# Kernel tuning notes

Hardware: AMD Instinct MI355X
Metric: run time of the kernel (lower is better)

## Reference

```python
import jax, jax.numpy as jnp
import numpy as np

N = 20000
E = 320000
IN_DIM = 16
H = 128
HEADS = 4
NEG_SLOPE = 0.2  # GATv2Conv default
EPS_LN = 1e-5


def setup_inputs() -> dict:
    key = jax.random.key(0)
    ks = jax.random.split(key, 16)
    f32 = jnp.float32
    def rn(k, shape, scale):
        return jax.random.normal(k, shape, dtype=f32) * scale
    s_in = 1.0 / np.sqrt(IN_DIM)
    s_h = 1.0 / np.sqrt(H)
    s_4h = 1.0 / np.sqrt(4 * H)
    s_2h = 1.0 / np.sqrt(2 * H)
    inp = {}
    inp["x"] = jax.random.normal(ks[0], (N, IN_DIM), dtype=f32)
    inp["edge_index"] = jax.random.randint(ks[1], (2, E), 0, N)
    inp["edge_attr"] = jax.random.normal(ks[2], (E, 2), dtype=f32)
    inp["emb_w"] = rn(ks[3], (IN_DIM, H), s_in)
    inp["emb_b"] = jnp.zeros((H,), f32)
    # 3 GATv2 layers stacked on leading axis
    inp["lin_l"] = rn(ks[4], (3, H, HEADS * H), s_h)
    inp["lin_r"] = rn(ks[5], (3, H, HEADS * H), s_h)
    inp["lin_edge"] = rn(ks[6], (3, 2, HEADS * H), 1.0 / np.sqrt(2.0))
    inp["att"] = rn(ks[7], (3, HEADS, H), s_h)
    inp["conv_bias01"] = jnp.zeros((2, HEADS * H), f32)  # concat=True layers
    inp["conv_bias2"] = jnp.zeros((H,), f32)             # concat=False layer
    inp["proj_w"] = rn(ks[8], (2, HEADS * H, H), s_4h)
    inp["proj_b"] = jnp.zeros((2, H), f32)
    inp["n1_g"] = jnp.ones((3, H), f32)
    inp["n1_b"] = jnp.zeros((3, H), f32)
    inp["n2_g"] = jnp.ones((3, H), f32)
    inp["n2_b"] = jnp.zeros((3, H), f32)
    inp["ffn_w1"] = rn(ks[9], (3, H, 2 * H), s_h)
    inp["ffn_b1"] = jnp.zeros((3, 2 * H), f32)
    inp["ffn_w2"] = rn(ks[10], (3, 2 * H, H), s_2h)
    inp["ffn_b2"] = jnp.zeros((3, H), f32)
    return inp


def layer_norm(x, g, b):
    mu = jnp.mean(x, axis=-1, keepdims=True)
    var = jnp.mean((x - mu) ** 2, axis=-1, keepdims=True)
    return (x - mu) * jax.lax.rsqrt(var + EPS_LN) * g + b


def gatv2(h, src, dst, eattr, Wl, Wr, We, att, bias, concat, n):
    # h: [n, H]; per-edge gather -> GATv2 attention -> segment softmax -> scatter-add
    xl = (h @ Wl).reshape(n, HEADS, H)   # source transform
    xr = (h @ Wr).reshape(n, HEADS, H)   # target transform
    ee = (eattr @ We).reshape(-1, HEADS, H)
    e = jax.nn.leaky_relu(xl[src] + xr[dst] + ee, NEG_SLOPE)  # [E', HEADS, H]
    score = jnp.einsum('ehc,hc->eh', e, att)                  # [E', HEADS]
    smax = jax.ops.segment_max(score, dst, num_segments=n)
    p = jnp.exp(score - smax[dst])
    denom = jax.ops.segment_sum(p, dst, num_segments=n)
    alpha = p / (denom[dst] + 1e-16)
    out = jax.ops.segment_sum(xl[src] * alpha[..., None], dst, num_segments=n)
    if concat:
        return out.reshape(n, HEADS * H) + bias
    return jnp.mean(out, axis=1) + bias


def reference(x, edge_index, edge_attr, emb_w, emb_b, lin_l, lin_r, lin_edge, att,
              conv_bias01, conv_bias2, proj_w, proj_b, n1_g, n1_b, n2_g, n2_b,
              ffn_w1, ffn_b1, ffn_w2, ffn_b2):
    n = x.shape[0]
    e = edge_attr.shape[0]
    # PyG add_self_loops with fill_value='mean': self-loop attr = mean of incoming edge attrs
    ones = jnp.ones((e,), x.dtype)
    deg = jax.ops.segment_sum(ones, edge_index[1], num_segments=n)
    loop_attr = jax.ops.segment_sum(edge_attr, edge_index[1], num_segments=n) / jnp.maximum(deg, 1.0)[:, None]
    ar = jnp.arange(n)
    src = jnp.concatenate([edge_index[0], ar])
    dst = jnp.concatenate([edge_index[1], ar])
    ea = jnp.concatenate([edge_attr, loop_attr], axis=0)

    h = x @ emb_w + emb_b
    for i in range(3):
        concat = i < 2
        bias = conv_bias01[i] if concat else conv_bias2
        h_in = h
        h = gatv2(h, src, dst, ea, lin_l[i], lin_r[i], lin_edge[i], att[i], bias, concat, n)
        if concat:
            h = h @ proj_w[i] + proj_b[i]
        h = layer_norm(h + h_in, n1_g[i], n1_b[i])
        h2 = h
        h = jax.nn.gelu(h @ ffn_w1[i] + ffn_b1[i], approximate=False) @ ffn_w2[i] + ffn_b2[i]
        h = layer_norm(h + h2, n2_g[i], n2_b[i])
    return h
```

## Files before the change

kernel.cpp:

```cpp
#include <hip/hip_runtime.h>
#include <math.h>

#define IN_DIM 16
#define HDIM   128
#define HEADS  4
#define HH     512
#define FFH    256
#define NEG_SLOPE 0.2f

typedef _Float16 half8 __attribute__((ext_vector_type(8)));
typedef _Float16 h8 __attribute__((ext_vector_type(8)));
typedef _Float16 h4 __attribute__((ext_vector_type(4)));
typedef _Float16 h2 __attribute__((ext_vector_type(2)));
typedef float f32x4 __attribute__((ext_vector_type(4)));

struct __align__(8) Edge { int src; _Float16 ea0, ea1; };

static __device__ inline float hsum8(h8 v) {
    h4 a = __builtin_shufflevector(v, v, 0, 1, 2, 3) +
           __builtin_shufflevector(v, v, 4, 5, 6, 7);
    h2 b = __builtin_shufflevector(a, a, 0, 1) +
           __builtin_shufflevector(a, a, 2, 3);
    return (float)b[0] + (float)b[1];
}

__global__ void xpad_kernel(const float* __restrict__ x, _Float16* __restrict__ xh, int n) {
    int idx = blockIdx.x * 256 + threadIdx.x;
    if (idx >= n * 64) return;
    int r = idx >> 6, k = idx & 63;
    xh[idx] = (k < IN_DIM) ? (_Float16)x[r * IN_DIM + k] : (_Float16)0.0f;
}

struct WDesc { const float* src; _Float16* dst; int Ksrc; int lgKd; int lgN; };
struct WDescs { WDesc d[15]; };
__global__ void wconv_kernel(WDescs ds) {
    WDesc w = ds.d[blockIdx.y];
    int Kd = 1 << w.lgKd;
    int total = 1 << (w.lgKd + w.lgN);
    for (int idx = blockIdx.x * 256 + threadIdx.x; idx < total; idx += gridDim.x * 256) {
        int n2 = idx >> w.lgKd, k = idx & (Kd - 1);
        w.dst[idx] = (k < w.Ksrc) ? (_Float16)w.src[(k << w.lgN) + n2] : (_Float16)0.0f;
    }
}

__global__ void wcvt_kernel(const float* __restrict__ we, const float* __restrict__ att,
                            const float* __restrict__ cb,
                            _Float16* __restrict__ weh, _Float16* __restrict__ atth,
                            _Float16* __restrict__ cbh) {
    int i = blockIdx.x * 256 + threadIdx.x;
    if (i < 3072) weh[i] = (_Float16)we[i];
    else if (i < 4608) atth[i - 3072] = (_Float16)att[i - 3072];
    else if (i < 5632) cbh[i - 4608] = (_Float16)cb[i - 4608];
}

__global__ void deg_kernel(const int* __restrict__ ei, const float* __restrict__ eattr,
                           float* deg, float* asum, int E) {
    int e = blockIdx.x * blockDim.x + threadIdx.x;
    if (e >= E) return;
    int d = ei[E + e];
    atomicAdd(&deg[d], 1.0f);
    atomicAdd(&asum[2 * d], eattr[2 * e]);
    atomicAdd(&asum[2 * d + 1], eattr[2 * e + 1]);
}

__global__ void scan_kernel(const float* __restrict__ deg, int* row_ptr, int* cur, int n) {
    __shared__ int sums[1024];
    int tid = threadIdx.x;
    int per = (n + 1023) / 1024;
    int s0 = tid * per;
    int s1 = s0 + per; if (s1 > n) s1 = n;
    int s = 0;
    for (int i = s0; i < s1; i++) s += (int)deg[i] + 1;
    int mysum = s;
    sums[tid] = s;
    __syncthreads();
    for (int dd = 1; dd < 1024; dd <<= 1) {
        int t = (tid >= dd) ? sums[tid - dd] : 0;
        __syncthreads();
        sums[tid] += t;
        __syncthreads();
    }
    int run = sums[tid] - mysum;
    for (int i = s0; i < s1; i++) {
        row_ptr[i] = run; cur[i] = run;
        run += (int)deg[i] + 1;
    }
    if (tid == 1023) row_ptr[n] = sums[1023];
}

__global__ void scatter_kernel(const int* __restrict__ ei, const float* __restrict__ eattr,
                               const float* __restrict__ deg, const float* __restrict__ asum,
                               int* cur, Edge* csr, int E, int n) {
    int i = blockIdx.x * blockDim.x + threadIdx.x;
    if (i >= E + n) return;
    Edge ed;
    int pos;
    if (i < E) {
        int d = ei[E + i];
        pos = atomicAdd(&cur[d], 1);
        ed.src = ei[i];
        ed.ea0 = (_Float16)eattr[2 * i];
        ed.ea1 = (_Float16)eattr[2 * i + 1];
    } else {
        int nd = i - E;
        float dv = fmaxf(deg[nd], 1.0f);
        pos = atomicAdd(&cur[nd], 1);
        ed.src = nd;
        ed.ea0 = (_Float16)(asum[2 * nd] / dv);
        ed.ea1 = (_Float16)(asum[2 * nd + 1] / dv);
    }
    csr[pos] = ed;
}

template <int KT, int OUTMODE>
__global__ __launch_bounds__(256) void gemm_bstat(const _Float16* __restrict__ A, int lda,
                                                  const _Float16* __restrict__ BT,
                                                  const float* __restrict__ bias,
                                                  float* __restrict__ C32,
                                                  _Float16* __restrict__ C16,
                                                  int M, int Nstride, int numMT) {
    const int PAD = 8, KC = KT / 32;
    __shared__ _Float16 Bs[128][KT + PAD];
    int tid = threadIdx.x;
    int wave = tid >> 6, lane = tid & 63;
    int quad = lane >> 4, l16 = lane & 15;
    int wrow = (wave >> 1) * 32, wcol = (wave & 1) * 64;
    int n0 = blockIdx.x * 128;

#pragma unroll
    for (int t = 0; t < KT / 16; t++) {
        int idx = tid + t * 256;
        int r = idx / (KT / 8), kb = (idx % (KT / 8)) * 8;
        *(half8*)&Bs[r][kb] = *(const half8*)(BT + (size_t)(n0 + r) * KT + kb);
    }
    __syncthreads();

    half8 bfrag[4][KC];
#pragma unroll
    for (int j = 0; j < 4; j++)
#pragma unroll
        for (int kc = 0; kc < KC; kc++)
            bfrag[j][kc] = *(const half8*)&Bs[wcol + j * 16 + l16][kc * 32 + quad * 8];

    float biasj[4];
#pragma unroll
    for (int j = 0; j < 4; j++)
        biasj[j] = bias ? bias[n0 + wcol + j * 16 + l16] : 0.0f;

    for (int mt = blockIdx.y; mt < numMT; mt += gridDim.y) {
        int rbase = mt * 64 + wrow;
        half8 af[2][KC];
#pragma unroll
        for (int i = 0; i < 2; i++) {
            int row = rbase + i * 16 + l16;
#pragma unroll
            for (int kc = 0; kc < KC; kc++)
                af[i][kc] = (row < M) ? *(const half8*)(A + (size_t)row * lda + kc * 32 + quad * 8)
                                      : (half8)(_Float16)0.0f;
        }
        f32x4 acc[2][4] = {};
#pragma unroll
        for (int kc = 0; kc < KC; kc++)
#pragma unroll
            for (int i = 0; i < 2; i++)
#pragma unroll
                for (int j = 0; j < 4; j++)
                    acc[i][j] = __builtin_amdgcn_mfma_f32_16x16x32_f16(af[i][kc], bfrag[j][kc], acc[i][j], 0, 0, 0);
#pragma unroll
        for (int i = 0; i < 2; i++) {
#pragma unroll
            for (int r = 0; r < 4; r++) {
                int row = rbase + i * 16 + quad * 4 + r;
                if (row >= M) continue;
#pragma unroll
                for (int j = 0; j < 4; j++) {
                    int col = n0 + wcol + j * 16 + l16;
                    float v = acc[i][j][r] + biasj[j];
                    if (OUTMODE == 2)
                        C32[(size_t)row * Nstride + col] = v;
                    C16[(size_t)row * Nstride + col] = (_Float16)v;
                }
            }
        }
    }
}

__global__ __launch_bounds__(256) void gemm_ln(const _Float16* __restrict__ A, int lda,
                                               const _Float16* __restrict__ BT,
                                               const float* __restrict__ bias,
                                               const float* __restrict__ R,
                                               const float* __restrict__ g,
                                               const float* __restrict__ b,
                                               float* __restrict__ C32,
                                               _Float16* __restrict__ C16,
                                               int M, int K) {
    const int BK = 64, PAD = 8;
    __shared__ _Float16 As[64][BK + PAD];
    __shared__ _Float16 Bs[128][BK + PAD];
    int tid = threadIdx.x;
    int wave = tid >> 6, lane = tid & 63;
    int quad = lane >> 4, l16 = lane & 15;
    int mBase = blockIdx.x * 64;

    f32x4 acc[8] = {};

    for (int k0 = 0; k0 < K; k0 += BK) {
#pragma unroll
        for (int t = 0; t < 2; t++) {
            int idx = tid + t * 256;
            int r = idx >> 3, kb = (idx & 7) * 8;
            half8 hv = {};
            int grow = mBase + r;
            if (grow < M) hv = *(const half8*)(A + (size_t)grow * lda + k0 + kb);
            *(half8*)&As[r][kb] = hv;
        }
#pragma unroll
        for (int t = 0; t < 4; t++) {
            int idx = tid + t * 256;
            int r = idx >> 3, kb = (idx & 7) * 8;
            *(half8*)&Bs[r][kb] = *(const half8*)(BT + (size_t)r * K + k0 + kb);
        }
        __syncthreads();
#pragma unroll
        for (int kc = 0; kc < 2; kc++) {
            half8 a = *(const half8*)&As[wave * 16 + l16][kc * 32 + quad * 8];
#pragma unroll
            for (int j = 0; j < 8; j++) {
                half8 bb = *(const half8*)&Bs[j * 16 + l16][kc * 32 + quad * 8];
                acc[j] = __builtin_amdgcn_mfma_f32_16x16x32_f16(a, bb, acc[j], 0, 0, 0);
            }
        }
        __syncthreads();
    }

    float gj[8], bj[8], biasj[8];
#pragma unroll
    for (int j = 0; j < 8; j++) {
        int col = j * 16 + l16;
        biasj[j] = bias[col];
        gj[j] = g[col];
        bj[j] = b[col];
    }
    int row0 = mBase + wave * 16 + quad * 4;
    float sum[4] = {}, sq[4] = {};
#pragma unroll
    for (int r = 0; r < 4; r++) {
        int row = row0 + r;
        bool ok = row < M;
        size_t base = (size_t)row * HDIM;
#pragma unroll
        for (int j = 0; j < 8; j++) {
            float v = acc[j][r] + biasj[j] + (ok ? R[base + j * 16 + l16] : 0.0f);
            acc[j][r] = v;
            sum[r] += v;
            sq[r] += v * v;
        }
    }
#pragma unroll
    for (int r = 0; r < 4; r++) {
#pragma unroll
        for (int off = 1; off < 16; off <<= 1) {
            sum[r] += __shfl_xor(sum[r], off);
            sq[r] += __shfl_xor(sq[r], off);
        }
    }
#pragma unroll
    for (int r = 0; r < 4; r++) {
        int row = row0 + r;
        if (row >= M) continue;
        size_t base = (size_t)row * HDIM;
        float mu = sum[r] * (1.0f / HDIM);
        float var = sq[r] * (1.0f / HDIM) - mu * mu;
        float invstd = rsqrtf(var + 1e-5f);
#pragma unroll
        for (int j = 0; j < 8; j++) {
            float o = (acc[j][r] - mu) * invstd * gj[j] + bj[j];
            C32[base + j * 16 + l16] = o;
            if (C16) C16[base + j * 16 + l16] = (_Float16)o;
        }
    }
}

__global__ __launch_bounds__(256) void ffn_fused(const _Float16* __restrict__ A,
                                                 const _Float16* __restrict__ W1T,
                                                 const float* __restrict__ b1,
                                                 const _Float16* __restrict__ W2T,
                                                 const float* __restrict__ b2,
                                                 const float* __restrict__ R,
                                                 const float* __restrict__ g,
                                                 const float* __restrict__ b,
                                                 float* __restrict__ C32,
                                                 _Float16* __restrict__ C16,
                                                 int M) {
    __shared__ _Float16 Ws[128][128 + 8];
    __shared__ _Float16 Mid[64][256 + 8];
    int tid = threadIdx.x;
    int wave = tid >> 6, lane = tid & 63;
    int quad = lane >> 4, l16 = lane & 15;
    int mBase = blockIdx.x * 64;

    half8 afrag[4];
    {
        int row = mBase + wave * 16 + l16;
#pragma unroll
        for (int kc = 0; kc < 4; kc++) {
            if (row < M)
                afrag[kc] = *(const half8*)(A + (size_t)row * HDIM + kc * 32 + quad * 8);
            else
                afrag[kc] = (half8)(_Float16)0.0f;
        }
    }

#pragma unroll
    for (int h = 0; h < 2; h++) {
        if (h) __syncthreads();
#pragma unroll
        for (int t = 0; t < 8; t++) {
            int idx = tid + t * 256;
            int r = idx >> 4, kb = (idx & 15) * 8;
            *(half8*)&Ws[r][kb] = *(const half8*)(W1T + (size_t)(h * 128 + r) * HDIM + kb);
        }
        __syncthreads();
        f32x4 acc[8] = {};
#pragma unroll
        for (int kc = 0; kc < 4; kc++) {
#pragma unroll
            for (int j = 0; j < 8; j++) {
                half8 bb = *(const half8*)&Ws[j * 16 + l16][kc * 32 + quad * 8];
                acc[j] = __builtin_amdgcn_mfma_f32_16x16x32_f16(afrag[kc], bb, acc[j], 0, 0, 0);
            }
        }
#pragma unroll
        for (int j = 0; j < 8; j++) {
            float bj1 = b1[h * 128 + j * 16 + l16];
#pragma unroll
            for (int r = 0; r < 4; r++) {
                float v = acc[j][r] + bj1;
                v = 0.5f * v * (1.0f + erff(v * 0.70710678118654752f));
                Mid[wave * 16 + quad * 4 + r][h * 128 + j * 16 + l16] = (_Float16)v;
            }
        }
    }
    __syncthreads();

    f32x4 acc2[8] = {};
#pragma unroll
    for (int kc2 = 0; kc2 < 2; kc2++) {
        if (kc2) __syncthreads();
#pragma unroll
        for (int t = 0; t < 8; t++) {
            int idx = tid + t * 256;
            int r = idx >> 4, kb = (idx & 15) * 8;
            *(half8*)&Ws[r][kb] = *(const half8*)(W2T + (size_t)r * FFH + kc2 * 128 + kb);
        }
        __syncthreads();
#pragma unroll
        for (int kc = 0; kc < 4; kc++) {
            half8 am = *(const half8*)&Mid[wave * 16 + l16][kc2 * 128 + kc * 32 + quad * 8];
#pragma unroll
            for (int j = 0; j < 8; j++) {
                half8 bb = *(const half8*)&Ws[j * 16 + l16][kc * 32 + quad * 8];
                acc2[j] = __builtin_amdgcn_mfma_f32_16x16x32_f16(am, bb, acc2[j], 0, 0, 0);
            }
        }
    }

    float gj[8], bj[8], b2j[8];
#pragma unroll
    for (int j = 0; j < 8; j++) {
        int col = j * 16 + l16;
        b2j[j] = b2[col];
        gj[j] = g[col];
        bj[j] = b[col];
    }
    int row0 = mBase + wave * 16 + quad * 4;
    float sum[4] = {}, sq[4] = {};
#pragma unroll
    for (int r = 0; r < 4; r++) {
        int row = row0 + r;
        bool ok = row < M;
        size_t base = (size_t)row * HDIM;
#pragma unroll
        for (int j = 0; j < 8; j++) {
            float v = acc2[j][r] + b2j[j] + (ok ? R[base + j * 16 + l16] : 0.0f);
            acc2[j][r] = v;
            sum[r] += v;
            sq[r] += v * v;
        }
    }
#pragma unroll
    for (int r = 0; r < 4; r++) {
#pragma unroll
        for (int off = 1; off < 16; off <<= 1) {
            sum[r] += __shfl_xor(sum[r], off);
            sq[r] += __shfl_xor(sq[r], off);
        }
    }
#pragma unroll
    for (int r = 0; r < 4; r++) {
        int row = row0 + r;
        if (row >= M) continue;
        size_t base = (size_t)row * HDIM;
        float mu = sum[r] * (1.0f / HDIM);
        float var = sq[r] * (1.0f / HDIM) - mu * mu;
        float invstd = rsqrtf(var + 1e-5f);
#pragma unroll
        for (int j = 0; j < 8; j++) {
            float o = (acc2[j][r] - mu) * invstd * gj[j] + bj[j];
            C32[base + j * 16 + l16] = o;
            if (C16) C16[base + j * 16 + l16] = (_Float16)o;
        }
    }
}

__global__ __launch_bounds__(256) void gat_edge_kernel(
    const _Float16* __restrict__ XLR,
    const int* __restrict__ row_ptr, const Edge* __restrict__ csr,
    const _Float16* __restrict__ WEH,
    const _Float16* __restrict__ ATTH,
    const _Float16* __restrict__ CBH,
    const float* __restrict__ cb2,
    _Float16* __restrict__ OUT16, float* __restrict__ OUT32,
    const float* __restrict__ R, const float* __restrict__ lng,
    const float* __restrict__ lnb, _Float16* __restrict__ OUT16h,
    int n, int concat) {
    __shared__ float sM[2][64], sL[2][64];
    __shared__ h8 sAcc[2][64];
    int tid = threadIdx.x;
    int wave = tid >> 6, lane = tid & 63;
    int nodeIdx = wave >> 1;
    int half = wave & 1;
    int node = blockIdx.x * 2 + nodeIdx;
    bool active = node < n;
    int c0 = lane * 8;

    h8 w08  = *(const h8*)(WEH + c0);
    h8 w18  = *(const h8*)(WEH + 512 + c0);
    h8 att8 = *(const h8*)(ATTH + c0);
    const _Float16 slope = (_Float16)NEG_SLOPE;

    h8 xr8 = (h8)(_Float16)0.0f;
    h8 acc2 = (h8)(_Float16)0.0f;
    float m = -INFINITY, l = 0.0f;

    if (active) {
        xr8 = *(const h8*)(XLR + (((unsigned)node << 10) + 512 + c0));
        int beg = row_ptr[node], end = row_ptr[node + 1];
        int mid = beg + ((end - beg + 1) >> 1);
        int b0 = half ? mid : beg;
        int e0 = half ? end : mid;
        int j = b0;
        for (; j + 3 < e0; j += 4) {
            Edge eg0 = csr[j], eg1 = csr[j + 1], eg2 = csr[j + 2], eg3 = csr[j + 3];
            const h8 x0 = *(const h8*)(XLR + (((unsigned)eg0.src << 10) + c0));
            const h8 x1 = *(const h8*)(XLR + (((unsigned)eg1.src << 10) + c0));
            const h8 x2 = *(const h8*)(XLR + (((unsigned)eg2.src << 10) + c0));
            const h8 x3 = *(const h8*)(XLR + (((unsigned)eg3.src << 10) + c0));
            h8 v0 = x0 + (xr8 + w08 * eg0.ea0 + w18 * eg0.ea1);
            h8 v1 = x1 + (xr8 + w08 * eg1.ea0 + w18 * eg1.ea1);
            h8 v2 = x2 + (xr8 + w08 * eg2.ea0 + w18 * eg2.ea1);
            h8 v3 = x3 + (xr8 + w08 * eg3.ea0 + w18 * eg3.ea1);
            v0 = __builtin_elementwise_max(v0, v0 * slope);
            v1 = __builtin_elementwise_max(v1, v1 * slope);
            v2 = __builtin_elementwise_max(v2, v2 * slope);
            v3 = __builtin_elementwise_max(v3, v3 * slope);
            float p0 = hsum8(v0 * att8);
            float p1 = hsum8(v1 * att8);
            float p2 = hsum8(v2 * att8);
            float p3 = hsum8(v3 * att8);
#pragma unroll
            for (int off = 1; off < 16; off <<= 1) {
                p0 += __shfl_xor(p0, off);
                p1 += __shfl_xor(p1, off);
                p2 += __shfl_xor(p2, off);
                p3 += __shfl_xor(p3, off);
            }
            float mnew = fmaxf(m, fmaxf(fmaxf(p0, p1), fmaxf(p2, p3)));
            float sc  = __expf(m - mnew);
            float e0f = __expf(p0 - mnew);
            float e1f = __expf(p1 - mnew);
            float e2f = __expf(p2 - mnew);
            float e3f = __expf(p3 - mnew);
            l = l * sc + ((e0f + e1f) + (e2f + e3f));
            acc2 = acc2 * (_Float16)sc
                 + (x0 * (_Float16)e0f + x1 * (_Float16)e1f)
                 + (x2 * (_Float16)e2f + x3 * (_Float16)e3f);
            m = mnew;
        }
        for (; j < e0; j++) {
            Edge eg0 = csr[j];
            const h8 x0 = *(const h8*)(XLR + (((unsigned)eg0.src << 10) + c0));
            h8 v0 = x0 + (xr8 + w08 * eg0.ea0 + w18 * eg0.ea1);
            v0 = __builtin_elementwise_max(v0, v0 * slope);
            float p0 = hsum8(v0 * att8);
            p0 += __shfl_xor(p0, 1);
            p0 += __shfl_xor(p0, 2);
            p0 += __shfl_xor(p0, 4);
            p0 += __shfl_xor(p0, 8);
            float mnew = fmaxf(m, p0);
            float sc = __expf(m - mnew);
            float e0f = __expf(p0 - mnew);
            l = l * sc + e0f;
            acc2 = acc2 * (_Float16)sc + x0 * (_Float16)e0f;
            m = mnew;
        }
    }

    if (half == 1) {
        sM[nodeIdx][lane] = m;
        sL[nodeIdx][lane] = l;
        sAcc[nodeIdx][lane] = acc2;
    }
    __syncthreads();
    if (half != 0 || !active) return;
    {
        float mB = sM[nodeIdx][lane];
        float lB = sL[nodeIdx][lane];
        h8 accB = sAcc[nodeIdx][lane];
        float mS = fmaxf(m, mB);
        float sA = __expf(m - mS);
        float sB = __expf(mB - mS);
        l = l * sA + lB * sB;
        acc2 = acc2 * (_Float16)sA + accB * (_Float16)sB;
    }

    float invf = 1.0f / (l + 1e-16f);
    if (concat) {
        h8 cb8 = *(const h8*)(CBH + c0);
        h8 o = acc2 * (_Float16)invf + cb8;
        *(h8*)(OUT16 + (((unsigned)node << 10) + c0)) = o;
    } else {
        float o8[8];
#pragma unroll
        for (int k = 0; k < 8; k++) {
            float a = (float)acc2[k] * invf;
            a += __shfl_xor(a, 16);
            a += __shfl_xor(a, 32);
            o8[k] = a;
        }
        float v8[8];
        float sum = 0.0f, sq = 0.0f;
        if (lane < 16) {
#pragma unroll
            for (int k = 0; k < 8; k++) {
                float v = o8[k] * 0.25f + cb2[c0 + k] + R[(size_t)node * HDIM + c0 + k];
                v8[k] = v;
                sum += v;
                sq += v * v;
            }
        }
#pragma unroll
        for (int off = 1; off < 16; off <<= 1) {
            sum += __shfl_xor(sum, off);
            sq += __shfl_xor(sq, off);
        }
        if (lane < 16) {
            float mu = sum * (1.0f / HDIM);
            float var = sq * (1.0f / HDIM) - mu * mu;
            float invstd = rsqrtf(var + 1e-5f);
#pragma unroll
            for (int k = 0; k < 8; k++) {
                float o = (v8[k] - mu) * invstd * lng[c0 + k] + lnb[c0 + k];
                OUT32[(size_t)node * HDIM + c0 + k] = o;
                OUT16h[(size_t)node * HDIM + c0 + k] = (_Float16)o;
            }
        }
    }
}

extern "C" void kernel_launch(void* const* d_in, const int* in_sizes, int n_in,
                              void* d_out, int out_size, void* d_ws, size_t ws_size,
                              hipStream_t stream) {
    const float* x        = (const float*)d_in[0];
    const int*   ei       = (const int*)d_in[1];
    const float* eattr    = (const float*)d_in[2];
    const float* emb_w    = (const float*)d_in[3];
    const float* emb_b    = (const float*)d_in[4];
    const float* lin_l    = (const float*)d_in[5];
    const float* lin_r    = (const float*)d_in[6];
    const float* lin_edge = (const float*)d_in[7];
    const float* attw     = (const float*)d_in[8];
    const float* cb01     = (const float*)d_in[9];
    const float* cb2      = (const float*)d_in[10];
    const float* proj_w   = (const float*)d_in[11];
    const float* proj_b   = (const float*)d_in[12];
    const float* n1g      = (const float*)d_in[13];
    const float* n1b      = (const float*)d_in[14];
    const float* n2g      = (const float*)d_in[15];
    const float* n2b      = (const float*)d_in[16];
    const float* fw1      = (const float*)d_in[17];
    const float* fb1      = (const float*)d_in[18];
    const float* fw2      = (const float*)d_in[19];
    const float* fb2      = (const float*)d_in[20];
    float* out = (float*)d_out;

    const int n = in_sizes[0] / IN_DIM;
    const int E = in_sizes[2] / 2;
    const int EP = E + n;
    const int numMT = (n + 63) / 64;

    size_t off = 0;
    auto alloc = [&](size_t bytes) {
        void* p = (char*)d_ws + off;
        off += (bytes + 255) & ~(size_t)255;
        return p;
    };
    float* deg     = (float*)alloc((size_t)n * 4);
    float* asum    = (float*)alloc((size_t)2 * n * 4);
    int*   row_ptr = (int*)alloc((size_t)(n + 1) * 4);
    int*   cur     = (int*)alloc((size_t)n * 4);
    Edge*  csr     = (Edge*)alloc((size_t)EP * 8);
    float* H0      = (float*)alloc((size_t)n * HDIM * 4);
    float* H1      = (float*)alloc((size_t)n * HDIM * 4);
    _Float16* H0h  = (_Float16*)alloc((size_t)n * HDIM * 2);
    _Float16* H1h  = (_Float16*)alloc((size_t)n * HDIM * 2);
    _Float16* XLR  = (_Float16*)alloc((size_t)n * 1024 * 2);
    _Float16* xh   = (_Float16*)alloc((size_t)n * 64 * 2);
    _Float16* wt_emb  = (_Float16*)alloc((size_t)HDIM * 64 * 2);
    _Float16* wt_llr  = (_Float16*)alloc((size_t)3 * 1024 * HDIM * 2);
    _Float16* wt_proj = (_Float16*)alloc((size_t)2 * HDIM * HH * 2);
    _Float16* wt_f1   = (_Float16*)alloc((size_t)3 * FFH * HDIM * 2);
    _Float16* wt_f2   = (_Float16*)alloc((size_t)3 * HDIM * FFH * 2);
    _Float16* weh     = (_Float16*)alloc((size_t)3 * 1024 * 2);
    _Float16* atth    = (_Float16*)alloc((size_t)3 * 512 * 2);
    _Float16* cbh     = (_Float16*)alloc((size_t)2 * 512 * 2);
    (void)ws_size;

    xpad_kernel<<<(n * 64 + 255) / 256, 256, 0, stream>>>(x, xh, n);
    WDescs ds;
    int di = 0;
    ds.d[di++] = {emb_w, wt_emb, IN_DIM, 6, 7};
    for (int i = 0; i < 3; i++) {
        ds.d[di++] = {lin_l + (size_t)i * HDIM * HH, wt_llr + (size_t)i * 1024 * HDIM, HDIM, 7, 9};
        ds.d[di++] = {lin_r + (size_t)i * HDIM * HH, wt_llr + (size_t)i * 1024 * HDIM + (size_t)512 * HDIM, HDIM, 7, 9};
    }
    for (int i = 0; i < 2; i++)
        ds.d[di++] = {proj_w + (size_t)i * HH * HDIM, wt_proj + (size_t)i * HDIM * HH, HH, 9, 7};
    for (int i = 0; i < 3; i++)
        ds.d[di++] = {fw1 + (size_t)i * HDIM * FFH, wt_f1 + (size_t)i * FFH * HDIM, HDIM, 7, 8};
    for (int i = 0; i < 3; i++)
        ds.d[di++] = {fw2 + (size_t)i * FFH * HDIM, wt_f2 + (size_t)i * HDIM * FFH, FFH, 8, 7};
    wconv_kernel<<<dim3(32, 15), 256, 0, stream>>>(ds);
    wcvt_kernel<<<22, 256, 0, stream>>>(lin_edge, attw, cb01, weh, atth, cbh);

    (void)hipMemsetAsync(deg, 0, (size_t)n * 4, stream);
    (void)hipMemsetAsync(asum, 0, (size_t)2 * n * 4, stream);
    deg_kernel<<<(E + 255) / 256, 256, 0, stream>>>(ei, eattr, deg, asum, E);
    scan_kernel<<<1, 1024, 0, stream>>>(deg, row_ptr, cur, n);
    scatter_kernel<<<(EP + 255) / 256, 256, 0, stream>>>(ei, eattr, deg, asum, cur, csr, E, n);

    gemm_bstat<64, 2><<<dim3(1, numMT), 256, 0, stream>>>(
        xh, 64, wt_emb, emb_b, H0, H0h, n, HDIM, numMT);

    for (int i = 0; i < 3; i++) {
        int concat = (i < 2);
        gemm_bstat<128, 1><<<dim3(8, 80), 256, 0, stream>>>(
            H0h, HDIM, wt_llr + (size_t)i * 1024 * HDIM, nullptr,
            nullptr, XLR, n, 1024, numMT);
        gat_edge_kernel<<<(n + 1) / 2, 256, 0, stream>>>(
            XLR, row_ptr, csr,
            weh + (size_t)i * 1024, atth + (size_t)i * 512,
            concat ? (cbh + (size_t)i * 512) : nullptr, cb2,
            XLR + 512, H1,
            H0, n1g + (size_t)i * HDIM, n1b + (size_t)i * HDIM, H1h,
            n, concat);
        if (concat) {
            gemm_ln<<<(n + 63) / 64, 256, 0, stream>>>(
                XLR + 512, 1024, wt_proj + (size_t)i * HDIM * HH,
                proj_b + (size_t)i * HDIM, H0,
                n1g + (size_t)i * HDIM, n1b + (size_t)i * HDIM,
                H1, H1h, n, HH);
        }
        float* lnout = (i == 2) ? out : H0;
        _Float16* lnout16 = (i == 2) ? nullptr : H0h;
        ffn_fused<<<(n + 63) / 64, 256, 0, stream>>>(
            H1h, wt_f1 + (size_t)i * FFH * HDIM, fb1 + (size_t)i * FFH,
            wt_f2 + (size_t)i * HDIM * FFH, fb2 + (size_t)i * HDIM, H1,
            n2g + (size_t)i * HDIM, n2b + (size_t)i * HDIM,
            lnout, lnout16, n);
    }
}
```

Measured before the change: 566.9 us.

## Process one node per wave with half-wave edge split and shuffle merge

The GAT edge kernel now assigns one node per wave instead of two waves per node. Each half-wave handles alternating edges, and every lane covers 16 channels rather than 8. The two partial online-softmax states are merged with cross-lane shuffles, which removes the shared-memory merge and the block barrier. This halves the grid size and cuts the per-edge shuffle-reduction steps. In exchange, each lane holds more registers, and the final layer-norm epilogue is rewritten with vectorised loads and stores.

```diff
diff --git a/kernel.cpp b/kernel.cpp
--- a/kernel.cpp
+++ b/kernel.cpp
@@ -13,6 +13,7 @@
 typedef _Float16 h4 __attribute__((ext_vector_type(4)));
 typedef _Float16 h2 __attribute__((ext_vector_type(2)));
 typedef float f32x4 __attribute__((ext_vector_type(4)));
+typedef int i32x4 __attribute__((ext_vector_type(4)));
 
 struct __align__(8) Edge { int src; _Float16 ea0, ea1; };
 
@@ -22,6 +23,16 @@
     h2 b = __builtin_shufflevector(a, a, 0, 1) +
            __builtin_shufflevector(a, a, 2, 3);
     return (float)b[0] + (float)b[1];
+}
+
+static __device__ inline h8 shfl_xor_h8(h8 v, int off) {
+    union { h8 h; i32x4 i; } u;
+    u.h = v;
+    u.i.x = __shfl_xor(u.i.x, off);
+    u.i.y = __shfl_xor(u.i.y, off);
+    u.i.z = __shfl_xor(u.i.z, off);
+    u.i.w = __shfl_xor(u.i.w, off);
+    return u.h;
 }
 
 __global__ void xpad_kernel(const float* __restrict__ x, _Float16* __restrict__ xh, int n) {
@@ -424,146 +435,177 @@
     const float* __restrict__ R, const float* __restrict__ lng,
     const float* __restrict__ lnb, _Float16* __restrict__ OUT16h,
     int n, int concat) {
-    __shared__ float sM[2][64], sL[2][64];
-    __shared__ h8 sAcc[2][64];
     int tid = threadIdx.x;
     int wave = tid >> 6, lane = tid & 63;
-    int nodeIdx = wave >> 1;
-    int half = wave & 1;
-    int node = blockIdx.x * 2 + nodeIdx;
-    bool active = node < n;
-    int c0 = lane * 8;
-
-    h8 w08  = *(const h8*)(WEH + c0);
-    h8 w18  = *(const h8*)(WEH + 512 + c0);
-    h8 att8 = *(const h8*)(ATTH + c0);
+    int g = lane >> 5;
+    int sub = lane & 31;
+    int node = blockIdx.x * 4 + wave;
+    if (node >= n) return;
+    int c0 = sub * 16;
+
+    h8 w0[2], w1[2], att[2], xr[2], acc[2];
+#pragma unroll
+    for (int k = 0; k < 2; k++) {
+        w0[k]  = *(const h8*)(WEH + c0 + k * 8);
+        w1[k]  = *(const h8*)(WEH + 512 + c0 + k * 8);
+        att[k] = *(const h8*)(ATTH + c0 + k * 8);
+        acc[k] = (h8)(_Float16)0.0f;
+    }
     const _Float16 slope = (_Float16)NEG_SLOPE;
 
-    h8 xr8 = (h8)(_Float16)0.0f;
-    h8 acc2 = (h8)(_Float16)0.0f;
-    float m = -INFINITY, l = 0.0f;
-
-    if (active) {
-        xr8 = *(const h8*)(XLR + (((unsigned)node << 10) + 512 + c0));
-        int beg = row_ptr[node], end = row_ptr[node + 1];
-        int mid = beg + ((end - beg + 1) >> 1);
-        int b0 = half ? mid : beg;
-        int e0 = half ? end : mid;
-        int j = b0;
-        for (; j + 3 < e0; j += 4) {
-            Edge eg0 = csr[j], eg1 = csr[j + 1], eg2 = csr[j + 2], eg3 = csr[j + 3];
-            const h8 x0 = *(const h8*)(XLR + (((unsigned)eg0.src << 10) + c0));
-            const h8 x1 = *(const h8*)(XLR + (((unsigned)eg1.src << 10) + c0));
-            const h8 x2 = *(const h8*)(XLR + (((unsigned)eg2.src << 10) + c0));
-            const h8 x3 = *(const h8*)(XLR + (((unsigned)eg3.src << 10) + c0));
-            h8 v0 = x0 + (xr8 + w08 * eg0.ea0 + w18 * eg0.ea1);
-            h8 v1 = x1 + (xr8 + w08 * eg1.ea0 + w18 * eg1.ea1);
-            h8 v2 = x2 + (xr8 + w08 * eg2.ea0 + w18 * eg2.ea1);
-            h8 v3 = x3 + (xr8 + w08 * eg3.ea0 + w18 * eg3.ea1);
-            v0 = __builtin_elementwise_max(v0, v0 * slope);
-            v1 = __builtin_elementwise_max(v1, v1 * slope);
-            v2 = __builtin_elementwise_max(v2, v2 * slope);
-            v3 = __builtin_elementwise_max(v3, v3 * slope);
-            float p0 = hsum8(v0 * att8);
-            float p1 = hsum8(v1 * att8);
-            float p2 = hsum8(v2 * att8);
-            float p3 = hsum8(v3 * att8);
-#pragma unroll
-            for (int off = 1; off < 16; off <<= 1) {
-                p0 += __shfl_xor(p0, off);
-                p1 += __shfl_xor(p1, off);
-                p2 += __shfl_xor(p2, off);
-                p3 += __shfl_xor(p3, off);
-            }
-            float mnew = fmaxf(m, fmaxf(fmaxf(p0, p1), fmaxf(p2, p3)));
-            float sc  = __expf(m - mnew);
-            float e0f = __expf(p0 - mnew);
-            float e1f = __expf(p1 - mnew);
-            float e2f = __expf(p2 - mnew);
-            float e3f = __expf(p3 - mnew);
-            l = l * sc + ((e0f + e1f) + (e2f + e3f));
-            acc2 = acc2 * (_Float16)sc
-                 + (x0 * (_Float16)e0f + x1 * (_Float16)e1f)
-                 + (x2 * (_Float16)e2f + x3 * (_Float16)e3f);
-            m = mnew;
-        }
-        for (; j < e0; j++) {
-            Edge eg0 = csr[j];
-            const h8 x0 = *(const h8*)(XLR + (((unsigned)eg0.src << 10) + c0));
-            h8 v0 = x0 + (xr8 + w08 * eg0.ea0 + w18 * eg0.ea1);
-            v0 = __builtin_elementwise_max(v0, v0 * slope);
-            float p0 = hsum8(v0 * att8);
-            p0 += __shfl_xor(p0, 1);
-            p0 += __shfl_xor(p0, 2);
-            p0 += __shfl_xor(p0, 4);
-            p0 += __shfl_xor(p0, 8);
-            float mnew = fmaxf(m, p0);
-            float sc = __expf(m - mnew);
-            float e0f = __expf(p0 - mnew);
-            l = l * sc + e0f;
-            acc2 = acc2 * (_Float16)sc + x0 * (_Float16)e0f;
-            m = mnew;
-        }
-    }
-
-    if (half == 1) {
-        sM[nodeIdx][lane] = m;
-        sL[nodeIdx][lane] = l;
-        sAcc[nodeIdx][lane] = acc2;
-    }
-    __syncthreads();
-    if (half != 0 || !active) return;
     {
-        float mB = sM[nodeIdx][lane];
-        float lB = sL[nodeIdx][lane];
-        h8 accB = sAcc[nodeIdx][lane];
-        float mS = fmaxf(m, mB);
+        unsigned nb = ((unsigned)node << 10) + 512u + (unsigned)c0;
+        xr[0] = *(const h8*)(XLR + nb);
+        xr[1] = *(const h8*)(XLR + nb + 8);
+    }
+
+    float m = -1e30f, l = 0.0f;
+    int beg = row_ptr[node], end = row_ptr[node + 1];
+    int e = beg + g;
+
+    for (; e + 2 < end; e += 4) {
+        Edge eg0 = csr[e], eg1 = csr[e + 2];
+        unsigned r0 = ((unsigned)eg0.src << 10) + (unsigned)c0;
+        unsigned r1 = ((unsigned)eg1.src << 10) + (unsigned)c0;
+        h8 x0a = *(const h8*)(XLR + r0);
+        h8 x0b = *(const h8*)(XLR + r0 + 8);
+        h8 x1a = *(const h8*)(XLR + r1);
+        h8 x1b = *(const h8*)(XLR + r1 + 8);
+
+        h8 v;
+        h8 p80, p81;
+        v = x0a + (xr[0] + w0[0] * eg0.ea0 + w1[0] * eg0.ea1);
+        v = __builtin_elementwise_max(v, v * slope);
+        p80 = v * att[0];
+        v = x0b + (xr[1] + w0[1] * eg0.ea0 + w1[1] * eg0.ea1);
+        v = __builtin_elementwise_max(v, v * slope);
+        p80 += v * att[1];
+        v = x1a + (xr[0] + w0[0] * eg1.ea0 + w1[0] * eg1.ea1);
+        v = __builtin_elementwise_max(v, v * slope);
+        p81 = v * att[0];
+        v = x1b + (xr[1] + w0[1] * eg1.ea0 + w1[1] * eg1.ea1);
+        v = __builtin_elementwise_max(v, v * slope);
+        p81 += v * att[1];
+
+        float p0 = hsum8(p80);
+        float p1 = hsum8(p81);
+        p0 += __shfl_xor(p0, 1); p1 += __shfl_xor(p1, 1);
+        p0 += __shfl_xor(p0, 2); p1 += __shfl_xor(p1, 2);
+        p0 += __shfl_xor(p0, 4); p1 += __shfl_xor(p1, 4);
+
+        float mnew = fmaxf(m, fmaxf(p0, p1));
+        float sc  = __expf(m - mnew);
+        float e0f = __expf(p0 - mnew);
+        float e1f = __expf(p1 - mnew);
+        l = l * sc + e0f + e1f;
+        _Float16 hs = (_Float16)sc, h0 = (_Float16)e0f, h1 = (_Float16)e1f;
+        acc[0] = acc[0] * hs + x0a * h0 + x1a * h1;
+        acc[1] = acc[1] * hs + x0b * h0 + x1b * h1;
+        m = mnew;
+    }
+    for (; e < end; e += 2) {
+        Edge eg0 = csr[e];
+        unsigned r0 = ((unsigned)eg0.src << 10) + (unsigned)c0;
+        h8 x0a = *(const h8*)(XLR + r0);
+        h8 x0b = *(const h8*)(XLR + r0 + 8);
+        h8 v;
+        h8 p80;
+        v = x0a + (xr[0] + w0[0] * eg0.ea0 + w1[0] * eg0.ea1);
+        v = __builtin_elementwise_max(v, v * slope);
+        p80 = v * att[0];
+        v = x0b + (xr[1] + w0[1] * eg0.ea0 + w1[1] * eg0.ea1);
+        v = __builtin_elementwise_max(v, v * slope);
+        p80 += v * att[1];
+        float p0 = hsum8(p80);
+        p0 += __shfl_xor(p0, 1);
+        p0 += __shfl_xor(p0, 2);
+        p0 += __shfl_xor(p0, 4);
+        float mnew = fmaxf(m, p0);
+        float sc  = __expf(m - mnew);
+        float e0f = __expf(p0 - mnew);
+        l = l * sc + e0f;
+        _Float16 hs = (_Float16)sc, h0 = (_Float16)e0f;
+        acc[0] = acc[0] * hs + x0a * h0;
+        acc[1] = acc[1] * hs + x0b * h0;
+        m = mnew;
+    }
+
+    {
+        float m2 = __shfl_xor(m, 32);
+        float l2 = __shfl_xor(l, 32);
+        h8 a20 = shfl_xor_h8(acc[0], 32);
+        h8 a21 = shfl_xor_h8(acc[1], 32);
+        float mS = fmaxf(m, m2);
         float sA = __expf(m - mS);
-        float sB = __expf(mB - mS);
-        l = l * sA + lB * sB;
-        acc2 = acc2 * (_Float16)sA + accB * (_Float16)sB;
+        float sB = __expf(m2 - mS);
+        l = l * sA + l2 * sB;
+        _Float16 hA = (_Float16)sA, hB = (_Float16)sB;
+        acc[0] = acc[0] * hA + a20 * hB;
+        acc[1] = acc[1] * hA + a21 * hB;
     }
 
     float invf = 1.0f / (l + 1e-16f);
     if (concat) {
-        h8 cb8 = *(const h8*)(CBH + c0);
-        h8 o = acc2 * (_Float16)invf + cb8;
-        *(h8*)(OUT16 + (((unsigned)node << 10) + c0)) = o;
+        _Float16 hi = (_Float16)invf;
+        h8 o0 = acc[0] * hi + *(const h8*)(CBH + c0);
+        h8 o1 = acc[1] * hi + *(const h8*)(CBH + c0 + 8);
+        if (g == 0) {
+            unsigned ob = ((unsigned)node << 10) + (unsigned)c0;
+            *(h8*)(OUT16 + ob) = o0;
+            *(h8*)(OUT16 + ob + 8) = o1;
+        }
     } else {
-        float o8[8];
-#pragma unroll
-        for (int k = 0; k < 8; k++) {
-            float a = (float)acc2[k] * invf;
-            a += __shfl_xor(a, 16);
-            a += __shfl_xor(a, 32);
-            o8[k] = a;
-        }
-        float v8[8];
-        float sum = 0.0f, sq = 0.0f;
-        if (lane < 16) {
-#pragma unroll
-            for (int k = 0; k < 8; k++) {
-                float v = o8[k] * 0.25f + cb2[c0 + k] + R[(size_t)node * HDIM + c0 + k];
-                v8[k] = v;
-                sum += v;
-                sq += v * v;
+        _Float16 hi = (_Float16)invf;
+        h8 t0 = acc[0] * hi;
+        h8 t1 = acc[1] * hi;
+        t0 = t0 + shfl_xor_h8(t0, 8);
+        t1 = t1 + shfl_xor_h8(t1, 8);
+        t0 = t0 + shfl_xor_h8(t0, 16);
+        t1 = t1 + shfl_xor_h8(t1, 16);
+        if (g == 0 && sub < 8) {
+            int d0 = sub * 16;
+            const float* Rp = R + (size_t)node * HDIM + d0;
+            const float* cp = cb2 + d0;
+            float v[16];
+            float sum = 0.0f, sq = 0.0f;
+#pragma unroll
+            for (int q = 0; q < 4; q++) {
+                f32x4 rv = *(const f32x4*)(Rp + q * 4);
+                f32x4 cv = *(const f32x4*)(cp + q * 4);
+#pragma unroll
+                for (int t = 0; t < 4; t++) {
+                    int k2 = q * 4 + t;
+                    float base = (k2 < 8) ? (float)t0[k2 & 7] : (float)t1[k2 & 7];
+                    float vv = base * 0.25f + cv[t] + rv[t];
+                    v[k2] = vv;
+                    sum += vv;
+                    sq += vv * vv;
+                }
             }
-        }
-#pragma unroll
-        for (int off = 1; off < 16; off <<= 1) {
-            sum += __shfl_xor(sum, off);
-            sq += __shfl_xor(sq, off);
-        }
-        if (lane < 16) {
+            sum += __shfl_xor(sum, 1); sq += __shfl_xor(sq, 1);
+            sum += __shfl_xor(sum, 2); sq += __shfl_xor(sq, 2);
+            sum += __shfl_xor(sum, 4); sq += __shfl_xor(sq, 4);
             float mu = sum * (1.0f / HDIM);
             float var = sq * (1.0f / HDIM) - mu * mu;
             float invstd = rsqrtf(var + 1e-5f);
-#pragma unroll
-            for (int k = 0; k < 8; k++) {
-                float o = (v8[k] - mu) * invstd * lng[c0 + k] + lnb[c0 + k];
-                OUT32[(size_t)node * HDIM + c0 + k] = o;
-                OUT16h[(size_t)node * HDIM + c0 + k] = (_Float16)o;
+            float* op = OUT32 + (size_t)node * HDIM + d0;
+            _Float16* oh = OUT16h + (size_t)node * HDIM + d0;
+            _Float16 o16[16];
+#pragma unroll
+            for (int q = 0; q < 4; q++) {
+                f32x4 gv = *(const f32x4*)(lng + d0 + q * 4);
+                f32x4 bv = *(const f32x4*)(lnb + d0 + q * 4);
+                f32x4 ov;
+#pragma unroll
+                for (int t = 0; t < 4; t++) {
+                    float o = (v[q * 4 + t] - mu) * invstd * gv[t] + bv[t];
+                    ov[t] = o;
+                    o16[q * 4 + t] = (_Float16)o;
+                }
+                *(f32x4*)(op + q * 4) = ov;
             }
+            *(h8*)(oh) = *(h8*)&o16[0];
+            *(h8*)(oh + 8) = *(h8*)&o16[8];
         }
     }
 }
@@ -657,7 +699,7 @@
         gemm_bstat<128, 1><<<dim3(8, 80), 256, 0, stream>>>(
             H0h, HDIM, wt_llr + (size_t)i * 1024 * HDIM, nullptr,
             nullptr, XLR, n, 1024, numMT);
-        gat_edge_kernel<<<(n + 1) / 2, 256, 0, stream>>>(
+        gat_edge_kernel<<<(n + 3) / 4, 256, 0, stream>>>(
             XLR, row_ptr, csr,
             weh + (size_t)i * 1024, atth + (size_t)i * 512,
             concat ? (cbh + (size_t)i * 512) : nullptr, cb2,
```

New measurement: 564.6 us. About the same (-0.4%).
